# Kernel tuning notes

Measured on AMD Instinct MI355X. Metric: run time of the kernel, lower is better.

Reference implementation:

```python
import math
import jax, jax.numpy as jnp
import numpy as np

ROUNDS = 4
BUCKET_LEN = 64
NEG_BIG = -1e9
NEG_SELF = -1e5
EPS = 1e-12


def look_back(x):
    # x: [B, n_buckets, bucket_len, ...]; prepend previous bucket (circular) along bucket_len axis
    return jnp.concatenate([jnp.roll(x, 1, axis=1), x], axis=2)


def gather_dim1(x, idx):
    # torch expand_gather: broadcast x and idx to common shape, gather along axis 1
    shape = np.broadcast_shapes(x.shape, idx.shape)
    return jnp.take_along_axis(jnp.broadcast_to(x, shape), jnp.broadcast_to(idx, shape), axis=1)


def setup_inputs() -> dict:
    key = jax.random.key(0)
    k1, k2, k3 = jax.random.split(key, 3)
    B, L, d_k = 16, 4096, 64
    n_buckets = L // BUCKET_LEN
    query = jax.random.normal(k1, (B, L, d_k), dtype=jnp.float32)
    value = jax.random.normal(k2, (B, L, d_k), dtype=jnp.float32)
    rand_matrix = jax.random.normal(k3, (B, d_k, ROUNDS, n_buckets // 2), dtype=jnp.float32)
    return {"query": query, "value": value, "rand_matrix": rand_matrix, "seed": 0}


def lsh_hashes(query, rand_matrix):
    # LocalitySensitiveHash.forward
    B, L, d_k = query.shape
    qn = query / jnp.maximum(jnp.linalg.norm(query, axis=-1, keepdims=True), EPS)
    rm = rand_matrix / jnp.linalg.norm(rand_matrix, axis=1, keepdims=True)
    mm = jnp.einsum('bld,bdrn->blrn', qn, rm)  # [B, L, rounds, n_buckets//2]
    h = jnp.argmax(jnp.concatenate([mm, -mm], axis=-1), axis=-1).astype(jnp.int32)  # [B, L, rounds]
    return h * L + jnp.arange(L, dtype=jnp.int32)[None, :, None]  # unique per position


def _lsh_attention(query, value, rand_matrix):
    B, L, d_k = query.shape
    R, bl = ROUNDS, BUCKET_LEN
    nb = L // bl

    h = lsh_hashes(query, rand_matrix)
    sorted_hashes = jnp.sort(h, axis=1)
    hash_indice = jnp.argsort(h, axis=1)               # [B, L, R]
    original_indice = jnp.argsort(hash_indice, axis=1)  # reverse_sort

    # reorder queries by hash, bucketize: [B, nb, bl, d_k, R]
    rq = gather_dim1(query[:, :, :, None], hash_indice[:, :, None, :]).reshape(B, nb, bl, d_k, R)
    lb_key = look_back(rq)
    lb_key = lb_key / jnp.maximum(jnp.linalg.norm(lb_key, axis=-2, keepdims=True), EPS)
    scores = jnp.einsum('bnidr,bnjdr->bnijr', rq, lb_key) / math.sqrt(d_k)  # [B, nb, bl, 2bl, R]

    # mask: different buckets, causal, self
    sh = sorted_hashes.reshape(B, nb, bl, R) // L  # bucket id
    scores = jnp.where(sh[..., None, :] != look_back(sh)[..., None, :, :], NEG_BIG, scores)
    qi = hash_indice.reshape(B, nb, bl, R).astype(jnp.int32)
    ki = look_back(qi)  # [B, nb, 2bl, R]
    scores = jnp.where(qi[..., None, :] < ki[..., None, :, :], NEG_BIG, scores)
    scores = jnp.where(qi[..., None, :] == ki[..., None, :, :], NEG_SELF, scores)

    # duplicate-key counting across rounds (get_dup_keys)
    ki_full = jnp.broadcast_to(ki[:, :, None, :, :], (B, nb, bl, 2 * bl, R)).reshape(B, L, 2 * bl, R)
    ki_full = gather_dim1(ki_full, original_indice[:, :, None, :])
    flat = ki_full.reshape(B, L, 2 * bl * R)
    s_idx = jnp.argsort(flat, axis=-1)
    s = jnp.take_along_axis(flat, s_idx, axis=-1)
    counts = jnp.ones_like(s)
    for i in range(1, R):
        eq = (s[..., i:] == s[..., :-i]).astype(s.dtype)
        counts = counts + jnp.pad(eq, ((0, 0), (0, 0), (i, 0))) + jnp.pad(eq, ((0, 0), (0, 0), (0, i)))
    inv = jnp.argsort(s_idx, axis=-1)
    count_key = jnp.take_along_axis(counts, inv, axis=-1).reshape(B, L, 2 * bl, R)
    count_key = gather_dim1(count_key, hash_indice[:, :, None, :])

    # duplicate-adjusted softmax
    scores = scores.reshape(B, L, 2 * bl, R)
    lse = jax.nn.logsumexp(scores, axis=2)  # [B, L, R]
    softmax_qk = jnp.exp(scores - jnp.log(count_key.astype(scores.dtype)) - lse[:, :, None, :])

    rv = gather_dim1(value[:, :, :, None], hash_indice[:, :, None, :]).reshape(B, nb, bl, d_k, R)
    sm = softmax_qk.reshape(B, nb, bl, 2 * bl, R)
    attn = jnp.einsum('bnijr,bnjdr->bnidr', sm, look_back(rv)).reshape(B, L, d_k, R)
    attn = gather_dim1(attn, original_indice[:, :, None, :])
    lse = jnp.take_along_axis(lse, original_indice, axis=1)
    round_weights = jax.nn.softmax(lse, axis=1)  # dim=1 (length) exactly as in the source
    return jnp.einsum('bldr,blr->bld', attn, round_weights)


def reference(query, value, rand_matrix, seed):
    # seed is unused by the original forward body; dropout skipped (eval mode)
    return _lsh_attention(query, value, rand_matrix)
```

## Files before the change

kernel.cpp:

```cpp
#include <hip/hip_runtime.h>
#include <math.h>

#define B_  16
#define L_  4096
#define D_  64
#define R_  4
#define NB_ 64
#define BL_ 64
#define FIXCAP 8192

typedef _Float16 f16x8 __attribute__((ext_vector_type(8)));
typedef _Float16 f16x2 __attribute__((ext_vector_type(2)));
typedef float    f32x4 __attribute__((ext_vector_type(4)));


__global__ __launch_bounds__(256, 4) void k_hash(const float* __restrict__ q,
                                                 const float* __restrict__ value,
                                                 const float* __restrict__ rm,
                                                 int* __restrict__ h_ws,
                                                 int* __restrict__ fix_cnt,
                                                 int* __restrict__ fix_list,
                                                 float* __restrict__ qscale_g,
                                                 _Float16* __restrict__ khf,
                                                 _Float16* __restrict__ vhf) {
    __shared__ __align__(16) char smem[36864];
    _Float16* Rhi = (_Float16*)smem;
    _Float16* Rlo = (_Float16*)(smem + 18432);
    float*    Sc  = (float*)smem;

    int blk = blockIdx.x;
    int b = blk >> 6, chunk = blk & 63;
    int tid = threadIdx.x;
    int w = tid >> 6, lane = tid & 63, quad = lane >> 4, l15 = lane & 15;

    {
        int row = chunk * 64 + (tid >> 2), sub = tid & 3;
        const float4* vp = (const float4*)(value + ((size_t)(b * L_ + row)) * 64 + sub * 16);
        f16x8 h0, h1;
        #pragma unroll
        for (int c = 0; c < 2; c++) {
            float4 t0 = vp[2 * c], t1 = vp[2 * c + 1];
            f16x8& hd = c ? h1 : h0;
            hd[0]=(_Float16)t0.x; hd[1]=(_Float16)t0.y; hd[2]=(_Float16)t0.z; hd[3]=(_Float16)t0.w;
            hd[4]=(_Float16)t1.x; hd[5]=(_Float16)t1.y; hd[6]=(_Float16)t1.z; hd[7]=(_Float16)t1.w;
        }
        _Float16* dst = vhf + ((size_t)(b * L_ + row)) * 64 + sub * 16;
        *(f16x8*)dst = h0;
        *(f16x8*)(dst + 8) = h1;
    }

    {
        int row = tid >> 1, dh2 = (tid & 1) * 32;
        int rr = row >> 5, nn = row & 31;
        const float* rpb = rm + (size_t)b * 8192 + rr * 32 + nn;
        float ss = 0.f;
        #pragma unroll
        for (int g = 0; g < 32; g++) { float v = rpb[(dh2 + g) * 128]; ss += v * v; }
        ss += __shfl_xor(ss, 1);
        float rn = 1.0f / sqrtf(ss);
        #pragma unroll
        for (int gg = 0; gg < 4; gg++) {
            f16x8 hv, lv;
            #pragma unroll
            for (int e = 0; e < 8; e++) {
                float f = rpb[(dh2 + gg * 8 + e) * 128] * rn;
                _Float16 h = (_Float16)f;
                hv[e] = h; lv[e] = (_Float16)(f - (float)h);
            }
            *(f16x8*)&Rhi[row * 72 + dh2 + gg * 8] = hv;
            *(f16x8*)&Rlo[row * 72 + dh2 + gg * 8] = lv;
        }
    }

    int qrow = chunk * 64 + w * 16 + l15;
    const float* qp = q + ((size_t)(b * L_ + qrow)) * 64;
    float qv[16];
    #pragma unroll
    for (int kt = 0; kt < 2; kt++) {
        float4 t0 = *(const float4*)(qp + kt * 32 + quad * 8);
        float4 t1 = *(const float4*)(qp + kt * 32 + quad * 8 + 4);
        qv[8*kt+0]=t0.x; qv[8*kt+1]=t0.y; qv[8*kt+2]=t0.z; qv[8*kt+3]=t0.w;
        qv[8*kt+4]=t1.x; qv[8*kt+5]=t1.y; qv[8*kt+6]=t1.z; qv[8*kt+7]=t1.w;
    }
    f16x8 Ahi[2], Alo[2];
    #pragma unroll
    for (int kt = 0; kt < 2; kt++) {
        #pragma unroll
        for (int j = 0; j < 8; j++) {
            _Float16 hi = (_Float16)qv[8*kt+j];
            Ahi[kt][j] = hi;
            Alo[kt][j] = (_Float16)(qv[8*kt+j] - (float)hi);
        }
    }
    {
        float ss = 0.f;
        #pragma unroll
        for (int j = 0; j < 16; j++) ss += qv[j] * qv[j];
        ss += __shfl_xor(ss, 16);
        ss += __shfl_xor(ss, 32);
        float nr = sqrtf(ss); if (nr < 1e-12f) nr = 1e-12f;
        float kscale = 0.18033688f / nr;
        if (quad == 0) qscale_g[(size_t)b * L_ + qrow] = nr * 5.5451774445f;
        _Float16* kd = khf + ((size_t)(b * L_ + qrow)) * 64;
        #pragma unroll
        for (int kt = 0; kt < 2; kt++) {
            f16x8 hv;
            #pragma unroll
            for (int j = 0; j < 8; j++) hv[j] = (_Float16)(qv[8*kt+j] * kscale);
            *(f16x8*)(kd + kt * 32 + quad * 8) = hv;
        }
    }
    __syncthreads();

    f32x4 acc[8];
    #pragma unroll
    for (int jt = 0; jt < 8; jt++) acc[jt] = (f32x4){0.f, 0.f, 0.f, 0.f};
    #pragma unroll
    for (int jt = 0; jt < 8; jt++) {
        #pragma unroll
        for (int kt = 0; kt < 2; kt++) {
            f16x8 bh = *(const f16x8*)&Rhi[(jt * 16 + l15) * 72 + kt * 32 + quad * 8];
            f16x8 bl = *(const f16x8*)&Rlo[(jt * 16 + l15) * 72 + kt * 32 + quad * 8];
            acc[jt] = __builtin_amdgcn_mfma_f32_16x16x32_f16(Ahi[kt], bh, acc[jt], 0, 0, 0);
            acc[jt] = __builtin_amdgcn_mfma_f32_16x16x32_f16(Ahi[kt], bl, acc[jt], 0, 0, 0);
            acc[jt] = __builtin_amdgcn_mfma_f32_16x16x32_f16(Alo[kt], bh, acc[jt], 0, 0, 0);
        }
    }
    __syncthreads();

    #pragma unroll
    for (int jt = 0; jt < 8; jt++) {
        #pragma unroll
        for (int reg = 0; reg < 4; reg++)
            Sc[(w * 16 + quad * 4 + reg) * 133 + jt * 16 + l15] = acc[jt][reg];
    }
    __syncthreads();

    {
        int row = tid & 63, r = tid >> 6;
        const float* sp = &Sc[row * 133 + r * 32];
        float v1 = -1e30f, v2 = -1e30f; int i1 = 0;
        #pragma unroll
        for (int n = 0; n < 32; n++) {
            float v = sp[n];
            float a = fabsf(v);
            int cand = n | ((__float_as_uint(v) >> 26) & 32);
            if (a > v1) i1 = cand;
            v2 = __builtin_amdgcn_fmed3f(a, v1, v2);
            v1 = fmaxf(a, v1);
        }
        int l = chunk * 64 + row;
        h_ws[((size_t)(b * 4 + r)) * L_ + l] = i1;
        if (v1 - v2 < 4e-5f) {
            int slot = atomicAdd(fix_cnt, 1);
            if (slot < FIXCAP) fix_list[slot] = (b << 14) | (r << 12) | l;
        }
    }
}

__global__ __launch_bounds__(64) void k_fix(const float* __restrict__ q,
                                            const float* __restrict__ rm,
                                            const int* __restrict__ fix_cnt,
                                            const int* __restrict__ fix_list,
                                            int* __restrict__ h_ws) {
    int cnt = *fix_cnt; if (cnt > FIXCAP) cnt = FIXCAP;
    int lane = threadIdx.x;
    for (int i = blockIdx.x; i < cnt; i += gridDim.x) {
        int e = fix_list[i];
        int b = e >> 14, r = (e >> 12) & 3, l = e & 4095;
        int n = lane & 31;
        const float* rpb = rm + (size_t)b * 8192 + r * 32 + n;
        const float* qr = q + ((size_t)(b * L_ + l)) * 64;
        double s2 = 0.0, dot = 0.0;
        #pragma unroll 8
        for (int d = 0; d < 64; d++) {
            double m = (double)rpb[d * 128];
            s2 += m * m;
            dot += (double)qr[d] * m;
        }
        double acc = dot / sqrt(s2);
        double v = (lane < 32) ? acc : -acc;
        int idx = lane;
        #pragma unroll
        for (int off = 1; off < 64; off <<= 1) {
            double ov = __shfl_xor(v, off);
            int   oidx = __shfl_xor(idx, off);
            if (ov > v || (ov == v && oidx < idx)) { v = ov; idx = oidx; }
        }
        if (lane == 0) h_ws[((size_t)(b * 4 + r)) * L_ + l] = idx;
    }
}

__global__ __launch_bounds__(256) void k_sort(const int* __restrict__ h_ws,
                                              int* __restrict__ oi_ws,
                                              int2* __restrict__ metaA) {
    __shared__ __align__(16) unsigned short cnt[64 * 257];
    __shared__ __align__(16) unsigned short oi_s[256 * 17];
    __shared__ __align__(16) unsigned short p_s[4096];
    __shared__ __align__(16) unsigned short sb_s[4096];
    __shared__ int part[256];
    __shared__ int bstart_s[64];

    int br = blockIdx.x;
    int t = threadIdx.x;
    const int* hp = h_ws + (size_t)br * L_;

    unsigned int* cz = (unsigned int*)cnt;
    #pragma unroll
    for (int i = 0; i < 33; i++) {
        int idx = i * 256 + t;
        if (idx < 8224) cz[idx] = 0;
    }

    int key[16];
    const int4* hp4 = (const int4*)(hp + t * 16);
    #pragma unroll
    for (int g = 0; g < 4; g++) {
        int4 v = hp4[g];
        key[g*4+0] = v.x; key[g*4+1] = v.y; key[g*4+2] = v.z; key[g*4+3] = v.w;
    }
    __syncthreads();

    #pragma unroll
    for (int k = 0; k < 16; k++) {
        unsigned short* c = &cnt[key[k] * 257 + t];
        *c = (unsigned short)(*c + 1);
    }
    __syncthreads();

    int u = t & 63, s = t >> 6;
    {
        int run = 0;
        int base_idx = u * 257 + s * 64;
        #pragma unroll 16
        for (int i = 0; i < 64; i++) {
            int c = cnt[base_idx + i];
            cnt[base_idx + i] = (unsigned short)run;
            run += c;
        }
        part[s * 64 + u] = run;
    }
    __syncthreads();

    if (t < 64) {
        int p0 = part[t], p1 = part[64 + t], p2 = part[128 + t], p3 = part[192 + t];
        int tot = p0 + p1 + p2 + p3;
        int v = tot;
        #pragma unroll
        for (int off = 1; off < 64; off <<= 1) {
            int o = __shfl_up(v, off);
            if (t >= off) v += o;
        }
        int base = v - tot;
        bstart_s[t] = base;
        part[t]       = base;
        part[64 + t]  = base + p0;
        part[128 + t] = base + p0 + p1;
        part[192 + t] = base + p0 + p1 + p2;
    }
    __syncthreads();

    int sbase = s * 64;
    #pragma unroll
    for (int k = 0; k < 16; k++) {
        int uk = key[k];
        unsigned short* c = &cnt[uk * 257 + t];
        int pos = part[sbase + uk] + *c;
        *c = (unsigned short)(*c + 1);
        int idx = t * 16 + k;
        oi_s[(idx >> 4) * 17 + (idx & 15)] = (unsigned short)pos;
        p_s[pos]  = (unsigned short)idx;
        sb_s[pos] = (unsigned short)bstart_s[uk];
    }
    __syncthreads();

    int* op = oi_ws + (size_t)br * L_;
    int2* mp = metaA + (size_t)br * L_;
    #pragma unroll
    for (int k = 0; k < 16; k++) {
        int e = k * 256 + t;
        op[e] = (int)oi_s[(e >> 4) * 17 + (e & 15)];
        mp[e] = make_int2((int)sb_s[e], (int)p_s[e]);
    }
}

__global__ __launch_bounds__(256) void k_pack(const int* __restrict__ oi_ws,
                                              int2* __restrict__ packA) {
    int gid = blockIdx.x * 256 + threadIdx.x;
    int b = gid >> 12, p = gid & 4095;
    int pack = 0, packm1 = 0;
    #pragma unroll
    for (int r2 = 0; r2 < 4; r2++) {
        int o = oi_ws[((size_t)(b * 4 + r2)) * L_ + p];
        int bk = o >> 6;
        pack   |= bk << (8 * r2);
        packm1 |= ((bk + 63) & 63) << (8 * r2);
    }
    packA[gid] = make_int2(pack, packm1);
}

__global__ __launch_bounds__(256, 4) void k_attn(const float* __restrict__ qscale_g,
                                                 const _Float16* __restrict__ khf,
                                                 const _Float16* __restrict__ vhf,
                                                 const int2* __restrict__ metaA,
                                                 const int2* __restrict__ packA,
                                                 float* __restrict__ lse_ws,
                                                 _Float16* __restrict__ attn_ws) {
    __shared__ _Float16 Ksh[128 * 72];
    __shared__ _Float16 Vt[64 * 136];
    __shared__ int4 kmeta[128];

    int xcd = blockIdx.x & 7, slot = blockIdx.x >> 3;
    int b = xcd * 2 + (slot >> 8);
    int rem = slot & 255, n = rem >> 2, r = rem & 3;
    int tid = threadIdx.x;
    int w = tid >> 6, lane = tid & 63, quad = lane >> 4, l15 = lane & 15;
    int hibase = (b * 4 + r) * L_;
    const int2* mpA = metaA + hibase;
    int nprev = (n + 63) & 63;

    {
        int j = tid >> 1, dh = (tid & 1) * 32;
        int spos = (j < 64) ? (nprev * 64 + j) : (n * 64 + (j - 64));
        int2 ma = mpA[spos];
        const _Float16* src = khf + ((size_t)(b * L_ + ma.y)) * 64 + dh;
        f16x8 t0 = *(const f16x8*)(src);
        f16x8 t1 = *(const f16x8*)(src + 8);
        f16x8 t2 = *(const f16x8*)(src + 16);
        f16x8 t3 = *(const f16x8*)(src + 24);
        if (dh == 0) {
            int2 pk = packA[b * L_ + ma.y];
            kmeta[j] = make_int4(ma.x, ma.y, pk.x, pk.y);
        }
        *(f16x8*)&Ksh[j * 72 + dh + 0]  = t0;
        *(f16x8*)&Ksh[j * 72 + dh + 8]  = t1;
        *(f16x8*)&Ksh[j * 72 + dh + 16] = t2;
        *(f16x8*)&Ksh[j * 72 + dh + 24] = t3;
    }
    __syncthreads();

    {
        int m = tid >> 2, sub = tid & 3;
        int y0 = kmeta[2 * m].y, y1 = kmeta[2 * m + 1].y;
        const _Float16* v0 = vhf + ((size_t)(b * L_ + y0)) * 64 + sub * 16;
        const _Float16* v1 = vhf + ((size_t)(b * L_ + y1)) * 64 + sub * 16;
        f16x8 a00 = *(const f16x8*)v0, a01 = *(const f16x8*)(v0 + 8);
        f16x8 a10 = *(const f16x8*)v1, a11 = *(const f16x8*)(v1 + 8);
        #pragma unroll
        for (int d = 0; d < 8; d++) {
            f16x2 hv = { a00[d], a10[d] };
            *(f16x2*)&Vt[(sub * 16 + d) * 136 + 2 * m] = hv;
            f16x2 hw = { a01[d], a11[d] };
            *(f16x2*)&Vt[(sub * 16 + 8 + d) * 136 + 2 * m] = hw;
        }
    }

    f16x8 afr[2];
    afr[0] = *(const f16x8*)&Ksh[(64 + w * 16 + l15) * 72 + quad * 8];
    afr[1] = *(const f16x8*)&Ksh[(64 + w * 16 + l15) * 72 + 32 + quad * 8];

    int4 qm4[4]; int km4z[8]; float qs4[4];
    #pragma unroll
    for (int reg = 0; reg < 4; reg++) {
        qm4[reg] = kmeta[64 + w * 16 + quad * 4 + reg];
        qs4[reg] = qscale_g[(size_t)b * L_ + qm4[reg].y];
    }
    #pragma unroll
    for (int jt = 0; jt < 8; jt++) km4z[jt] = kmeta[jt * 16 + l15].z;

    f32x4 acc[8];
    #pragma unroll
    for (int jt = 0; jt < 8; jt++) acc[jt] = (f32x4){0.f, 0.f, 0.f, 0.f};
    __builtin_amdgcn_s_setprio(1);
    #pragma unroll
    for (int jt = 0; jt < 8; jt++) {
        #pragma unroll
        for (int kt = 0; kt < 2; kt++) {
            f16x8 bfr = *(const f16x8*)&Ksh[(jt * 16 + l15) * 72 + kt * 32 + quad * 8];
            acc[jt] = __builtin_amdgcn_mfma_f32_16x16x32_f16(afr[kt], bfr, acc[jt], 0, 0, 0);
        }
    }
    __builtin_amdgcn_s_setprio(0);
    __syncthreads();

    _Float16* Ph = Ksh;
    float lse_r[4], inv_r[4];
    #pragma unroll
    for (int reg = 0; reg < 4; reg++) {
        int lo = qm4[reg].x - (n - 1) * 64;
        int width = w * 16 + quad * 4 + reg + 64 - lo;
        int jl = l15 - lo;
        float qs = qs4[reg];
        float s[8];
        #pragma unroll
        for (int jt = 0; jt < 8; jt++) {
            float v = acc[jt][reg] * qs;
            int ju = jt * 16 + jl;
            v = ((unsigned)ju < (unsigned)width) ? v : -1.4426951e9f;
            if (ju == width) v = -144269.50f;
            s[jt] = v;
        }
        float m = s[0];
        #pragma unroll
        for (int jt = 1; jt < 8; jt++) m = fmaxf(m, s[jt]);
        #pragma unroll
        for (int off = 1; off < 16; off <<= 1) m = fmaxf(m, __shfl_xor(m, off));
        float te[8], sum = 0.f;
        #pragma unroll
        for (int jt = 0; jt < 8; jt++) { te[jt] = __builtin_amdgcn_exp2f(s[jt] - m); sum += te[jt]; }
        #pragma unroll
        for (int off = 1; off < 16; off <<= 1) sum += __shfl_xor(sum, off);
        inv_r[reg] = __builtin_amdgcn_rcpf(sum);
        lse_r[reg] = m * 0.6931472f + __logf(sum);
        int i = w * 16 + quad * 4 + reg;
        #pragma unroll
        for (int jt = 0; jt < 8; jt++) {
            int z1 = km4z[jt] ^ qm4[reg].z;
            int z2 = km4z[jt] ^ qm4[reg].w;
            int nz = __popc((z1 + 0x7f7f7f7f) & 0x80808080)
                   + __popc((z2 + 0x7f7f7f7f) & 0x80808080);
            float p = te[jt] * __builtin_amdgcn_rcpf((float)(8 - nz));
            Ph[i * 136 + jt * 16 + l15] = (_Float16)p;
        }
    }
    if (l15 == 0) {
        #pragma unroll
        for (int reg = 0; reg < 4; reg++)
            lse_ws[hibase + qm4[reg].y] = lse_r[reg];
    }
    __syncthreads();

    f32x4 oacc[4];
    #pragma unroll
    for (int nt = 0; nt < 4; nt++) oacc[nt] = (f32x4){0.f, 0.f, 0.f, 0.f};
    __builtin_amdgcn_s_setprio(1);
    #pragma unroll
    for (int kt = 0; kt < 4; kt++) {
        f16x8 pa = *(const f16x8*)&Ph[(w * 16 + l15) * 136 + kt * 32 + quad * 8];
        #pragma unroll
        for (int nt = 0; nt < 4; nt++) {
            f16x8 vb = *(const f16x8*)&Vt[(nt * 16 + l15) * 136 + kt * 32 + quad * 8];
            oacc[nt] = __builtin_amdgcn_mfma_f32_16x16x32_f16(pa, vb, oacc[nt], 0, 0, 0);
        }
    }
    __builtin_amdgcn_s_setprio(0);
    __syncthreads();

    _Float16* Pout = Ksh;
    #pragma unroll
    for (int nt = 0; nt < 4; nt++) {
        #pragma unroll
        for (int reg = 0; reg < 4; reg++) {
            int i = w * 16 + quad * 4 + reg;
            Pout[i * 72 + nt * 16 + l15] = (_Float16)(oacc[nt][reg] * inv_r[reg]);
        }
    }
    __syncthreads();

    {
        int row = tid >> 2, part = tid & 3;
        int y = kmeta[64 + row].y;
        _Float16* dst = attn_ws + ((size_t)hibase + y) * 64;
        f16x8 v0 = *(const f16x8*)&Pout[row * 72 + part * 8];
        f16x8 v1 = *(const f16x8*)&Pout[row * 72 + 32 + part * 8];
        *(f16x8*)(dst + part * 8) = v0;
        *(f16x8*)(dst + 32 + part * 8) = v1;
    }
}

__global__ __launch_bounds__(256) void k_rw(const float* __restrict__ lse_ws,
                                            float* __restrict__ rwmax,
                                            float* __restrict__ rwsum) {
    __shared__ float  red[256];
    __shared__ double redd[256];
    int br = blockIdx.x;
    const float* lp = lse_ws + (size_t)br * L_;
    int t = threadIdx.x;
    float m = -1e30f;
    for (int k = t; k < L_; k += 256) m = fmaxf(m, lp[k]);
    red[t] = m; __syncthreads();
    for (int s2 = 128; s2 > 0; s2 >>= 1) {
        if (t < s2) red[t] = fmaxf(red[t], red[t + s2]);
        __syncthreads();
    }
    float mm = red[0];
    double s = 0.0;
    for (int k = t; k < L_; k += 256) s += (double)expf(lp[k] - mm);
    redd[t] = s; __syncthreads();
    for (int s2 = 128; s2 > 0; s2 >>= 1) {
        if (t < s2) redd[t] += redd[t + s2];
        __syncthreads();
    }
    if (t == 0) { rwmax[br] = mm; rwsum[br] = (float)redd[0]; }
}

__global__ __launch_bounds__(256) void k_out(const _Float16* __restrict__ attn_ws,
                                             const float* __restrict__ lse_ws,
                                             const float* __restrict__ rwmax,
                                             const float* __restrict__ rwsum,
                                             float* __restrict__ out) {
    int gid = blockIdx.x * 256 + threadIdx.x;
    int g = gid & 7;
    size_t row = (size_t)(gid >> 3);
    int b = (int)(row >> 12), l = (int)(row & 4095);
    float o[8];
    #pragma unroll
    for (int k = 0; k < 8; k++) o[k] = 0.f;
    #pragma unroll
    for (int r = 0; r < 4; r++) {
        int br = b * 4 + r;
        float wgt = __expf(lse_ws[(size_t)br * L_ + l] - rwmax[br])
                  * __builtin_amdgcn_rcpf(rwsum[br]);
        f16x8 av = *(const f16x8*)&attn_ws[(((size_t)br * L_ + l) << 6) + g * 8];
        #pragma unroll
        for (int k = 0; k < 8; k++) o[k] += (float)av[k] * wgt;
    }
    float4* op = (float4*)(out + row * 64 + g * 8);
    op[0] = make_float4(o[0], o[1], o[2], o[3]);
    op[1] = make_float4(o[4], o[5], o[6], o[7]);
}

extern "C" void kernel_launch(void* const* d_in, const int* in_sizes, int n_in,
                              void* d_out, int out_size, void* d_ws, size_t ws_size,
                              hipStream_t stream) {
    const float* query = (const float*)d_in[0];
    const float* value = (const float*)d_in[1];
    const float* rm    = (const float*)d_in[2];
    char* ws = (char*)d_ws;
    int*       h_ws   = (int*)(ws + ((size_t)1 << 20));
    int*       oi_ws  = (int*)(ws + ((size_t)3 << 20));
    float*     lse_ws = (float*)(ws + ((size_t)4 << 20));
    float*     rwmax  = (float*)(ws + ((size_t)5 << 20));
    float*     rwsum  = (float*)(ws + ((size_t)5 << 20) + 256);
    int*       fix_cnt= (int*)(ws + ((size_t)5 << 20) + 512);
    int*       fix_list=(int*)(ws + ((size_t)5 << 20) + 1024);
    _Float16*  attn_ws= (_Float16*)(ws + ((size_t)6 << 20));
    int2*      metaA  = (int2*)(ws + ((size_t)41 << 20));
    int2*      packA  = (int2*)(ws + ((size_t)43 << 20));
    float*     qscale = (float*)(ws + ((size_t)45 << 20));
    _Float16*  khf    = (_Float16*)(ws + ((size_t)53 << 20));
    _Float16*  vhf    = (_Float16*)(ws + ((size_t)61 << 20));
    float*     out    = (float*)d_out;

    hipMemsetAsync(fix_cnt, 0, sizeof(int), stream);
    hipLaunchKernelGGL(k_hash,   dim3(1024), dim3(256), 0, stream, query, value, rm,
                       h_ws, fix_cnt, fix_list, qscale, khf, vhf);
    hipLaunchKernelGGL(k_fix,    dim3(64),   dim3(64),  0, stream, query, rm,
                       fix_cnt, fix_list, h_ws);
    hipLaunchKernelGGL(k_sort,   dim3(64),   dim3(256), 0, stream, h_ws, oi_ws, metaA);
    hipLaunchKernelGGL(k_pack,   dim3(256),  dim3(256), 0, stream, oi_ws, packA);
    hipLaunchKernelGGL(k_attn,   dim3(4096), dim3(256), 0, stream,
                       qscale, khf, vhf, metaA, packA, lse_ws, attn_ws);
    hipLaunchKernelGGL(k_rw,     dim3(64),   dim3(256), 0, stream, lse_ws, rwmax, rwsum);
    hipLaunchKernelGGL(k_out,    dim3(2048), dim3(256), 0, stream,
                       attn_ws, lse_ws, rwmax, rwsum, out);
}
```

Baseline: 160.1 us.

## Fold hash fixup and bucket packing into sort kernel, drop memset and two launches

```diff
diff --git a/kernel.cpp b/kernel.cpp
--- a/kernel.cpp
+++ b/kernel.cpp
@@ -7,7 +7,6 @@
 #define R_  4
 #define NB_ 64
 #define BL_ 64
-#define FIXCAP 8192
 
 typedef _Float16 f16x8 __attribute__((ext_vector_type(8)));
 typedef _Float16 f16x2 __attribute__((ext_vector_type(2)));
@@ -18,8 +17,6 @@
                                                  const float* __restrict__ value,
                                                  const float* __restrict__ rm,
                                                  int* __restrict__ h_ws,
-                                                 int* __restrict__ fix_cnt,
-                                                 int* __restrict__ fix_list,
                                                  float* __restrict__ qscale_g,
                                                  _Float16* __restrict__ khf,
                                                  _Float16* __restrict__ vhf) {
@@ -150,74 +147,94 @@
             v1 = fmaxf(a, v1);
         }
         int l = chunk * 64 + row;
+        if (v1 - v2 < 4e-5f) i1 |= (1 << 30);
         h_ws[((size_t)(b * 4 + r)) * L_ + l] = i1;
-        if (v1 - v2 < 4e-5f) {
-            int slot = atomicAdd(fix_cnt, 1);
-            if (slot < FIXCAP) fix_list[slot] = (b << 14) | (r << 12) | l;
-        }
     }
 }
 
-__global__ __launch_bounds__(64) void k_fix(const float* __restrict__ q,
-                                            const float* __restrict__ rm,
-                                            const int* __restrict__ fix_cnt,
-                                            const int* __restrict__ fix_list,
-                                            int* __restrict__ h_ws) {
-    int cnt = *fix_cnt; if (cnt > FIXCAP) cnt = FIXCAP;
-    int lane = threadIdx.x;
-    for (int i = blockIdx.x; i < cnt; i += gridDim.x) {
-        int e = fix_list[i];
-        int b = e >> 14, r = (e >> 12) & 3, l = e & 4095;
-        int n = lane & 31;
-        const float* rpb = rm + (size_t)b * 8192 + r * 32 + n;
-        const float* qr = q + ((size_t)(b * L_ + l)) * 64;
-        double s2 = 0.0, dot = 0.0;
-        #pragma unroll 8
-        for (int d = 0; d < 64; d++) {
-            double m = (double)rpb[d * 128];
-            s2 += m * m;
-            dot += (double)qr[d] * m;
-        }
-        double acc = dot / sqrt(s2);
-        double v = (lane < 32) ? acc : -acc;
-        int idx = lane;
-        #pragma unroll
-        for (int off = 1; off < 64; off <<= 1) {
-            double ov = __shfl_xor(v, off);
-            int   oidx = __shfl_xor(idx, off);
-            if (ov > v || (ov == v && oidx < idx)) { v = ov; idx = oidx; }
-        }
-        if (lane == 0) h_ws[((size_t)(b * 4 + r)) * L_ + l] = idx;
-    }
-}
-
 __global__ __launch_bounds__(256) void k_sort(const int* __restrict__ h_ws,
-                                              int* __restrict__ oi_ws,
-                                              int2* __restrict__ metaA) {
+                                              const float* __restrict__ q,
+                                              const float* __restrict__ rm,
+                                              int2* __restrict__ metaA,
+                                              unsigned char* __restrict__ packB) {
     __shared__ __align__(16) unsigned short cnt[64 * 257];
     __shared__ __align__(16) unsigned short oi_s[256 * 17];
     __shared__ __align__(16) unsigned short p_s[4096];
     __shared__ __align__(16) unsigned short sb_s[4096];
     __shared__ int part[256];
     __shared__ int bstart_s[64];
+    __shared__ int flcnt;
 
     int br = blockIdx.x;
+    int b = br >> 2, r = br & 3;
     int t = threadIdx.x;
     const int* hp = h_ws + (size_t)br * L_;
+
+    if (t == 0) flcnt = 0;
+
+    int key[16]; unsigned fmask = 0;
+    const int4* hp4 = (const int4*)(hp + t * 16);
+    #pragma unroll
+    for (int g = 0; g < 4; g++) {
+        int4 v = hp4[g];
+        int raw[4] = { v.x, v.y, v.z, v.w };
+        #pragma unroll
+        for (int j = 0; j < 4; j++) {
+            int k = g * 4 + j;
+            key[k] = raw[j] & 63;
+            if (raw[j] & (1 << 30)) fmask |= 1u << k;
+        }
+    }
+    __syncthreads();
+
+    if (fmask) {
+        #pragma unroll
+        for (int k = 0; k < 16; k++)
+            if (fmask & (1u << k)) {
+                int slot = atomicAdd(&flcnt, 1);
+                sb_s[slot] = (unsigned short)(t * 16 + k);
+            }
+    }
+    __syncthreads();
+
+    {
+        int wid = t >> 6, lane = t & 63;
+        int fc = flcnt;
+        for (int e = wid; e < fc; e += 4) {
+            int l = sb_s[e];
+            int n = lane & 31;
+            const float* rpb = rm + (size_t)b * 8192 + r * 32 + n;
+            const float* qr = q + ((size_t)(b * L_ + l)) * 64;
+            double s2 = 0.0, dot = 0.0;
+            for (int d = 0; d < 64; d++) {
+                double m = (double)rpb[d * 128];
+                s2 += m * m;
+                dot += (double)qr[d] * m;
+            }
+            double acc = dot / sqrt(s2);
+            double v = (lane < 32) ? acc : -acc;
+            int idx = lane;
+            #pragma unroll
+            for (int off = 1; off < 64; off <<= 1) {
+                double ov = __shfl_xor(v, off);
+                int   oidx = __shfl_xor(idx, off);
+                if (ov > v || (ov == v && oidx < idx)) { v = ov; idx = oidx; }
+            }
+            if (lane == 0) p_s[l] = (unsigned short)idx;
+        }
+    }
+    __syncthreads();
+    if (fmask) {
+        #pragma unroll
+        for (int k = 0; k < 16; k++)
+            if (fmask & (1u << k)) key[k] = p_s[t * 16 + k];
+    }
 
     unsigned int* cz = (unsigned int*)cnt;
     #pragma unroll
     for (int i = 0; i < 33; i++) {
         int idx = i * 256 + t;
         if (idx < 8224) cz[idx] = 0;
-    }
-
-    int key[16];
-    const int4* hp4 = (const int4*)(hp + t * 16);
-    #pragma unroll
-    for (int g = 0; g < 4; g++) {
-        int4 v = hp4[g];
-        key[g*4+0] = v.x; key[g*4+1] = v.y; key[g*4+2] = v.z; key[g*4+3] = v.w;
     }
     __syncthreads();
 
@@ -274,36 +291,22 @@
     }
     __syncthreads();
 
-    int* op = oi_ws + (size_t)br * L_;
     int2* mp = metaA + (size_t)br * L_;
+    unsigned char* pb = packB + ((size_t)b * L_) * 4 + r;
     #pragma unroll
     for (int k = 0; k < 16; k++) {
         int e = k * 256 + t;
-        op[e] = (int)oi_s[(e >> 4) * 17 + (e & 15)];
         mp[e] = make_int2((int)sb_s[e], (int)p_s[e]);
-    }
-}
-
-__global__ __launch_bounds__(256) void k_pack(const int* __restrict__ oi_ws,
-                                              int2* __restrict__ packA) {
-    int gid = blockIdx.x * 256 + threadIdx.x;
-    int b = gid >> 12, p = gid & 4095;
-    int pack = 0, packm1 = 0;
-    #pragma unroll
-    for (int r2 = 0; r2 < 4; r2++) {
-        int o = oi_ws[((size_t)(b * 4 + r2)) * L_ + p];
-        int bk = o >> 6;
-        pack   |= bk << (8 * r2);
-        packm1 |= ((bk + 63) & 63) << (8 * r2);
-    }
-    packA[gid] = make_int2(pack, packm1);
+        int pos = (int)oi_s[(e >> 4) * 17 + (e & 15)];
+        pb[(size_t)e * 4] = (unsigned char)(pos >> 6);
+    }
 }
 
 __global__ __launch_bounds__(256, 4) void k_attn(const float* __restrict__ qscale_g,
                                                  const _Float16* __restrict__ khf,
                                                  const _Float16* __restrict__ vhf,
                                                  const int2* __restrict__ metaA,
-                                                 const int2* __restrict__ packA,
+                                                 const unsigned int* __restrict__ packA,
                                                  float* __restrict__ lse_ws,
                                                  _Float16* __restrict__ attn_ws) {
     __shared__ _Float16 Ksh[128 * 72];
@@ -329,8 +332,9 @@
         f16x8 t2 = *(const f16x8*)(src + 16);
         f16x8 t3 = *(const f16x8*)(src + 24);
         if (dh == 0) {
-            int2 pk = packA[b * L_ + ma.y];
-            kmeta[j] = make_int4(ma.x, ma.y, pk.x, pk.y);
+            unsigned int pk = packA[b * L_ + ma.y];
+            unsigned int pm1 = ((pk | 0x40404040u) - 0x01010101u) & 0x3f3f3f3fu;
+            kmeta[j] = make_int4(ma.x, ma.y, (int)pk, (int)pm1);
         }
         *(f16x8*)&Ksh[j * 72 + dh + 0]  = t0;
         *(f16x8*)&Ksh[j * 72 + dh + 8]  = t1;
@@ -528,29 +532,23 @@
     const float* rm    = (const float*)d_in[2];
     char* ws = (char*)d_ws;
     int*       h_ws   = (int*)(ws + ((size_t)1 << 20));
-    int*       oi_ws  = (int*)(ws + ((size_t)3 << 20));
     float*     lse_ws = (float*)(ws + ((size_t)4 << 20));
     float*     rwmax  = (float*)(ws + ((size_t)5 << 20));
     float*     rwsum  = (float*)(ws + ((size_t)5 << 20) + 256);
-    int*       fix_cnt= (int*)(ws + ((size_t)5 << 20) + 512);
-    int*       fix_list=(int*)(ws + ((size_t)5 << 20) + 1024);
     _Float16*  attn_ws= (_Float16*)(ws + ((size_t)6 << 20));
     int2*      metaA  = (int2*)(ws + ((size_t)41 << 20));
-    int2*      packA  = (int2*)(ws + ((size_t)43 << 20));
+    unsigned char* packB = (unsigned char*)(ws + ((size_t)43 << 20));
     float*     qscale = (float*)(ws + ((size_t)45 << 20));
     _Float16*  khf    = (_Float16*)(ws + ((size_t)53 << 20));
     _Float16*  vhf    = (_Float16*)(ws + ((size_t)61 << 20));
     float*     out    = (float*)d_out;
 
-    hipMemsetAsync(fix_cnt, 0, sizeof(int), stream);
     hipLaunchKernelGGL(k_hash,   dim3(1024), dim3(256), 0, stream, query, value, rm,
-                       h_ws, fix_cnt, fix_list, qscale, khf, vhf);
-    hipLaunchKernelGGL(k_fix,    dim3(64),   dim3(64),  0, stream, query, rm,
-                       fix_cnt, fix_list, h_ws);
-    hipLaunchKernelGGL(k_sort,   dim3(64),   dim3(256), 0, stream, h_ws, oi_ws, metaA);
-    hipLaunchKernelGGL(k_pack,   dim3(256),  dim3(256), 0, stream, oi_ws, packA);
+                       h_ws, qscale, khf, vhf);
+    hipLaunchKernelGGL(k_sort,   dim3(64),   dim3(256), 0, stream, h_ws, query, rm,
+                       metaA, packB);
     hipLaunchKernelGGL(k_attn,   dim3(4096), dim3(256), 0, stream,
-                       qscale, khf, vhf, metaA, packA, lse_ws, attn_ws);
+                       qscale, khf, vhf, metaA, (const unsigned int*)packB, lse_ws, attn_ws);
     hipLaunchKernelGGL(k_rw,     dim3(64),   dim3(256), 0, stream, lse_ws, rwmax, rwsum);
     hipLaunchKernelGGL(k_out,    dim3(2048), dim3(256), 0, stream,
                        attn_ws, lse_ws, rwmax, rwsum, out);
```

Result: faster. 156.0 us (-2.5%).
